# Kernel optimization log

Measured on AMD Instinct MI355X. Metric: run time of the kernel, lower is better.

## Reference

```python
import jax, jax.numpy as jnp
import numpy as np

B, L, DIM = 2, 1024, 512
HEADS = 8
D = DIM // HEADS
FORE_DIM, POST_DIM = 256, 1024
L_FORE, L_POST = 4 * L, L // 4


def setup_inputs() -> dict:
    key = jax.random.key(0)
    ks = jax.random.split(key, 8)
    s = 0.02  # weight init scale
    return {
        "x": jax.random.normal(ks[0], (B, L, DIM), jnp.float32),
        "fore_x": jax.random.normal(ks[1], (B, L_FORE, FORE_DIM), jnp.float32),
        "post_x": jax.random.normal(ks[2], (B, L_POST, POST_DIM), jnp.float32),
        # Linear weights stored [in, out] (transposed vs torch nn.Linear)
        "wq": jax.random.normal(ks[3], (DIM, DIM), jnp.float32) * s,
        "bq": jnp.zeros((DIM,), jnp.float32),
        "wkv1": jax.random.normal(ks[4], (FORE_DIM, 2 * DIM), jnp.float32) * s,
        "bkv1": jnp.zeros((2 * DIM,), jnp.float32),
        "wkv2": jax.random.normal(ks[5], (POST_DIM, 2 * DIM), jnp.float32) * s,
        "bkv2": jnp.zeros((2 * DIM,), jnp.float32),
        "wproj": jax.random.normal(ks[6], (3 * DIM, DIM), jnp.float32) * s,
        "bproj": jnp.zeros((DIM,), jnp.float32),
    }


def reference(x, fore_x, post_x, wq, bq, wkv1, bkv1, wkv2, bkv2, wproj, bproj):
    scale = D ** (-0.5)
    # q: [B, H, L, D], pre-scaled as in the torch code
    q = (x @ wq + bq).reshape(B, L, HEADS, D).transpose(0, 2, 1, 3) * scale

    def cross_attn(ctx, w, b):
        # ctx: [B, Lc, Cin] -> k, v: [B, H, Lc, D]
        kv = (ctx @ w + b).reshape(B, ctx.shape[1], 2, HEADS, D)
        k = kv[:, :, 0].transpose(0, 2, 1, 3)
        v = kv[:, :, 1].transpose(0, 2, 1, 3)
        attn = jax.nn.softmax(jnp.einsum("bhqd,bhkd->bhqk", q, k), axis=-1)
        out = jnp.einsum("bhqk,bhkd->bhqd", attn, v)
        return out.transpose(0, 2, 1, 3).reshape(B, L, DIM)

    x_2 = cross_attn(post_x, wkv2, bkv2)
    x_1 = cross_attn(fore_x, wkv1, bkv1)
    cat = jnp.concatenate([x, x_1, x_2], axis=2)  # [B, L, 3*DIM]
    return cat @ wproj + bproj
```

## Files before the change

kernel.cpp:

```cpp
#include <hip/hip_runtime.h>
#include <hip/hip_bf16.h>
#include <stdint.h>

typedef __attribute__((ext_vector_type(8))) short bf8;
typedef __attribute__((ext_vector_type(4))) short bf4;
typedef __attribute__((ext_vector_type(2))) short bf2;
typedef __attribute__((ext_vector_type(4))) float f32x4;

__device__ inline short f2bf(float f) {
  union { __hip_bfloat16 h; short s; } u;
  u.h = __float2bfloat16(f);
  return u.s;
}
__device__ inline float bf2f(short s) {
  union { short s; __hip_bfloat16 h; } u;
  u.s = s;
  return __bfloat162float(u.h);
}

__device__ inline f32x4 mfma16(bf8 a, bf8 b, f32x4 c) {
  return __builtin_amdgcn_mfma_f32_16x16x32_bf16(a, b, c, 0, 0, 0);
}

__global__ __launch_bounds__(256) void gemm3_k(
    const float* __restrict__ x, const float* __restrict__ fore,
    const float* __restrict__ post,
    const float* __restrict__ wq, const float* __restrict__ wkv1,
    const float* __restrict__ bkv1, const float* __restrict__ wkv2,
    short* __restrict__ kv1, short* __restrict__ cat,
    float* __restrict__ qpart, float* __restrict__ kv2part)
{
  __shared__ __align__(16) short a_lds[2][128 * 40];
  __shared__ __align__(16) short b_lds[2][64 * 40];

  const int bid = blockIdx.x;
  const float *A, *W, *bias = nullptr;
  void* out;
  int N, lda, ldo, m0, n0, koff;
  bool f32out, wcat = false;
  if (bid < 1024) {
    A = fore; W = wkv1; bias = bkv1; out = kv1;
    N = 1024; lda = 256; ldo = 1024; koff = 0;
    m0 = (bid >> 4) * 128; n0 = (bid & 15) * 64; f32out = false;
  } else if (bid < 1280) {
    int j = bid - 1024; int kc = j >> 7; j &= 127;
    A = x; W = wq; out = qpart + (size_t)kc * (2048 * 512);
    N = 512; lda = 512; ldo = 512; koff = kc * 256;
    m0 = (j >> 3) * 128; n0 = (j & 7) * 64; f32out = true;
    wcat = (j & 7) == 0;
  } else {
    int j = bid - 1280; int kc = j >> 6; j &= 63;
    A = post; W = wkv2; out = kv2part + (size_t)kc * (512 * 1024);
    N = 1024; lda = 1024; ldo = 1024; koff = kc * 256;
    m0 = (j >> 4) * 128; n0 = (j & 15) * 64; f32out = true;
  }

  const int tid = threadIdx.x;
  const int w = tid >> 6, lane = tid & 63, g = lane >> 4, lr = lane & 15;
  const int wrow = w & 1, wcol = w >> 1;

  f32x4 z = {0.f, 0.f, 0.f, 0.f};
  f32x4 acc[4][2];
#pragma unroll
  for (int mi = 0; mi < 4; ++mi)
#pragma unroll
    for (int ni = 0; ni < 2; ++ni) acc[mi][ni] = z;

  const int arow = tid >> 3, ac4 = tid & 7;
  const int bcol = tid & 63, bj4 = tid >> 6;

  float4 ra[4], rna[4];
  float rw[8], rnw[8];

  auto LOADA = [&](int kg, float4* af, float* wg) {
#pragma unroll
    for (int i = 0; i < 4; ++i)
      af[i] = *(const float4*)&A[(size_t)(m0 + arow + 32 * i) * lda + kg + ac4 * 4];
#pragma unroll
    for (int j = 0; j < 8; ++j)
      wg[j] = W[(size_t)(kg + bj4 * 8 + j) * N + n0 + bcol];
  };
  auto STAGE = [&](int b, const float4* af, const float* wg, int kg) {
#pragma unroll
    for (int i = 0; i < 4; ++i) {
      int rr = arow + 32 * i;
      int s = (ac4 >> 1) ^ (rr & 3);
      bf4 o;
      o[0] = f2bf(af[i].x); o[1] = f2bf(af[i].y);
      o[2] = f2bf(af[i].z); o[3] = f2bf(af[i].w);
      *(bf4*)&a_lds[b][rr * 40 + s * 8 + (ac4 & 1) * 4] = o;
      if (wcat)
        *(bf4*)&cat[(size_t)(m0 + rr) * 1536 + kg + ac4 * 4] = o;
    }
    int s = bj4 ^ (bcol & 3);
    bf8 o;
#pragma unroll
    for (int j = 0; j < 8; ++j) o[j] = f2bf(wg[j]);
    *(bf8*)&b_lds[b][bcol * 40 + s * 8] = o;
  };

  LOADA(koff, ra, rw);
  STAGE(0, ra, rw, koff);
  LOADA(koff + 32, rna, rnw);
  __syncthreads();

#pragma unroll
  for (int it = 0; it < 8; ++it) {
    if (it < 7) STAGE((it + 1) & 1, rna, rnw, koff + (it + 1) * 32);
    if (it < 6) LOADA(koff + (it + 2) * 32, rna, rnw);

    const int b = it & 1;
    bf8 afr[4], bfr[2];
#pragma unroll
    for (int mi = 0; mi < 4; ++mi) {
      int row = wrow * 64 + mi * 16 + lr;
      afr[mi] = *(const bf8*)&a_lds[b][row * 40 + ((g ^ (row & 3)) << 3)];
    }
#pragma unroll
    for (int ni = 0; ni < 2; ++ni) {
      int col = wcol * 32 + ni * 16 + lr;
      bfr[ni] = *(const bf8*)&b_lds[b][col * 40 + ((g ^ (col & 3)) << 3)];
    }
#pragma unroll
    for (int mi = 0; mi < 4; ++mi)
#pragma unroll
      for (int ni = 0; ni < 2; ++ni)
        acc[mi][ni] = mfma16(afr[mi], bfr[ni], acc[mi][ni]);
    __syncthreads();
  }

#pragma unroll
  for (int ni = 0; ni < 2; ++ni) {
    int col = n0 + wcol * 32 + ni * 16 + lr;
    float bv = f32out ? 0.f : bias[col];
#pragma unroll
    for (int mi = 0; mi < 4; ++mi) {
      int rowb = m0 + wrow * 64 + mi * 16 + g * 4;
#pragma unroll
      for (int r = 0; r < 4; ++r) {
        float val = acc[mi][ni][r] + bv;
        if (f32out)
          ((float*)out)[(size_t)(rowb + r) * ldo + col] = val;
        else
          ((short*)out)[(size_t)(rowb + r) * ldo + col] = f2bf(val);
      }
    }
  }
}

__global__ __launch_bounds__(256) void finalize_k(
    const float* __restrict__ qpart, const float* __restrict__ kv2part,
    const float* __restrict__ bq, const float* __restrict__ bkv2,
    short* __restrict__ qb, short* __restrict__ kv2)
{
  int i = blockIdx.x * 256 + threadIdx.x;
  if (i < 262144) {
    int col = (i * 4) & 511;
    float4 a = ((const float4*)qpart)[i];
    float4 b = ((const float4*)qpart)[i + 262144];
    float4 bv = *(const float4*)&bq[col];
    bf4 o;
    o[0] = f2bf((a.x + b.x + bv.x) * 0.125f);
    o[1] = f2bf((a.y + b.y + bv.y) * 0.125f);
    o[2] = f2bf((a.z + b.z + bv.z) * 0.125f);
    o[3] = f2bf((a.w + b.w + bv.w) * 0.125f);
    ((bf4*)qb)[i] = o;
  } else {
    int j = i - 262144;
    int col = (j * 4) & 1023;
    float4 a = ((const float4*)kv2part)[j];
    float4 b = ((const float4*)kv2part)[j + 131072];
    float4 c = ((const float4*)kv2part)[j + 262144];
    float4 d = ((const float4*)kv2part)[j + 393216];
    float4 bv = *(const float4*)&bkv2[col];
    bf4 o;
    o[0] = f2bf(a.x + b.x + c.x + d.x + bv.x);
    o[1] = f2bf(a.y + b.y + c.y + d.y + bv.y);
    o[2] = f2bf(a.z + b.z + c.z + d.z + bv.z);
    o[3] = f2bf(a.w + b.w + c.w + d.w + bv.w);
    ((bf4*)kv2)[j] = o;
  }
}

__global__ __launch_bounds__(256) void gemmo_k(
    const short* __restrict__ A, const float* __restrict__ W,
    const float* __restrict__ bias, float* __restrict__ out,
    int N, int K, int lda, int ldo)
{
  __shared__ __align__(16) short a_lds[2][64 * 40];
  __shared__ __align__(16) short b_lds[2][64 * 40];
  const int tid = threadIdx.x;
  const int w = tid >> 6, lane = tid & 63, g = lane >> 4, lr = lane & 15;
  const int m0 = blockIdx.x * 64, n0 = blockIdx.y * 64;

  f32x4 z = {0.f, 0.f, 0.f, 0.f};
  f32x4 acc[4];
#pragma unroll
  for (int mi = 0; mi < 4; ++mi) acc[mi] = z;

  const int arow = tid >> 2, ac8 = tid & 3;
  const int bcol = tid & 63, bj4 = tid >> 6;
  bf8 ra, rna;
  float rw[8], rnw[8];

  auto LOADA = [&](int kg, bf8& ab, float* wg) {
    ab = *(const bf8*)&A[(size_t)(m0 + arow) * lda + kg + ac8 * 8];
#pragma unroll
    for (int j = 0; j < 8; ++j)
      wg[j] = W[(size_t)(kg + bj4 * 8 + j) * N + n0 + bcol];
  };
  auto STAGE = [&](int b, bf8 ab, const float* wg) {
    *(bf8*)&a_lds[b][arow * 40 + ((ac8 ^ (arow & 3)) << 3)] = ab;
    int s = bj4 ^ (bcol & 3);
    bf8 o;
#pragma unroll
    for (int j = 0; j < 8; ++j) o[j] = f2bf(wg[j]);
    *(bf8*)&b_lds[b][bcol * 40 + s * 8] = o;
  };

  const int nit = K >> 5;
  LOADA(0, ra, rw);
  STAGE(0, ra, rw);
  LOADA(32, rna, rnw);
  __syncthreads();

  for (int it = 0; it < nit; ++it) {
    if (it + 1 < nit) STAGE((it + 1) & 1, rna, rnw);
    if (it + 2 < nit) LOADA((it + 2) * 32, rna, rnw);

    const int b = it & 1;
    bf8 afr[4], bfr;
#pragma unroll
    for (int mi = 0; mi < 4; ++mi) {
      int row = mi * 16 + lr;
      afr[mi] = *(const bf8*)&a_lds[b][row * 40 + ((g ^ (row & 3)) << 3)];
    }
    {
      int col = w * 16 + lr;
      bfr = *(const bf8*)&b_lds[b][col * 40 + ((g ^ (col & 3)) << 3)];
    }
#pragma unroll
    for (int mi = 0; mi < 4; ++mi) acc[mi] = mfma16(afr[mi], bfr, acc[mi]);
    __syncthreads();
  }

  {
    int col = n0 + w * 16 + lr;
    float bv = bias[col];
#pragma unroll
    for (int mi = 0; mi < 4; ++mi) {
      int rowb = m0 + mi * 16 + g * 4;
#pragma unroll
      for (int r = 0; r < 4; ++r)
        out[(size_t)(rowb + r) * ldo + col] = acc[mi][r] + bv;
    }
  }
}

__global__ __launch_bounds__(256) void attn_k(
    const short* __restrict__ q,
    const short* __restrict__ kv1, const short* __restrict__ kv2,
    short* __restrict__ o1, float* __restrict__ l1,
    short* __restrict__ o2, float* __restrict__ l2)
{
  __shared__ __align__(16) short k_lds[64 * 64];
  __shared__ __align__(16) short v_lds[64 * 72];
  const int tid = threadIdx.x;
  const int w = tid >> 6, lane = tid & 63, g = lane >> 4, lr = lane & 15;

  const int bid = blockIdx.x;
  const short* kvsrc;
  short* opart;
  float* lpart;
  int qt, h, bb, split, chunk, Lc;
  if (bid < 1024) {
    qt = bid & 7; h = (bid >> 3) & 7;
    int zz = bid >> 6; bb = zz >> 3; split = zz & 7;
    kvsrc = kv1; opart = o1; lpart = l1; chunk = 512; Lc = 4096;
  } else {
    int j = bid - 1024;
    qt = j & 7; h = (j >> 3) & 7;
    int zz = j >> 6; bb = zz >> 2; split = zz & 3;
    kvsrc = kv2; opart = o2; lpart = l2; chunk = 64; Lc = 256;
  }

  const int qbase = bb * 1024 + qt * 128 + w * 32;
  bf8 qfA[2], qfB[2];
#pragma unroll
  for (int s2 = 0; s2 < 2; ++s2) {
    const short* qp = &q[(size_t)(qbase + s2 * 16 + lr) * 512 + h * 64];
    qfA[s2] = *(const bf8*)&qp[g * 8];
    qfB[s2] = *(const bf8*)&qp[32 + g * 8];
  }

  const f32x4 z = {0.f, 0.f, 0.f, 0.f};
  f32x4 oaccT[2][4];
#pragma unroll
  for (int s2 = 0; s2 < 2; ++s2)
#pragma unroll
    for (int i = 0; i < 4; ++i) oaccT[s2][i] = z;
  float lsum_l[2] = {0.f, 0.f};

  const short* kvb = kvsrc + (size_t)bb * Lc * 1024 + (size_t)split * chunk * 1024;

  const int krow = tid >> 2, ksl = tid & 3;
  const short* kgp = kvb + (size_t)krow * 1024 + h * 64;
  const int vi = tid & 31, vj = tid >> 5;
  const short* vgp = kvb + (size_t)(2 * vi) * 1024 + 512 + h * 64 + vj * 8;
  const int lc0 = 2 * vi;
  const int vpos = (lc0 & 32) + ((lc0 & 12) << 1) + ((lc0 & 16) >> 2) + (lc0 & 3);

  bf8 k0c, k1c, v0c, v1c;
  k0c = *(const bf8*)(kgp + ksl * 8);
  k1c = *(const bf8*)(kgp + (ksl + 4) * 8);
  v0c = *(const bf8*)vgp;
  v1c = *(const bf8*)(vgp + 1024);

  const int nit = chunk >> 6;
  for (int it = 0; it < nit; ++it) {
    __syncthreads();
    *(bf8*)&k_lds[krow * 64 + ((ksl ^ (krow & 7)) << 3)] = k0c;
    *(bf8*)&k_lds[krow * 64 + (((ksl + 4) ^ (krow & 7)) << 3)] = k1c;
#pragma unroll
    for (int jj = 0; jj < 8; ++jj) {
      int d = vj * 8 + jj;
      bf2 pr; pr[0] = v0c[jj]; pr[1] = v1c[jj];
      *(bf2*)&v_lds[d * 72 + vpos] = pr;
    }
    __syncthreads();
    if (it + 1 < nit) {
      size_t off = (size_t)64 * 1024 * (it + 1);
      k0c = *(const bf8*)(kgp + off + ksl * 8);
      k1c = *(const bf8*)(kgp + off + (ksl + 4) * 8);
      v0c = *(const bf8*)(vgp + off);
      v1c = *(const bf8*)(vgp + off + 1024);
    }

    f32x4 sv[2][4];
#pragma unroll
    for (int t = 0; t < 4; ++t) {
      int lc = t * 16 + lr;
      bf8 kf0 = *(const bf8*)&k_lds[lc * 64 + ((g ^ (lc & 7)) << 3)];
      bf8 kf1 = *(const bf8*)&k_lds[lc * 64 + (((4 + g) ^ (lc & 7)) << 3)];
#pragma unroll
      for (int s2 = 0; s2 < 2; ++s2) {
        sv[s2][t] = mfma16(kf0, qfA[s2], z);
        sv[s2][t] = mfma16(kf1, qfB[s2], sv[s2][t]);
      }
    }

    bf8 pb[2][2];
#pragma unroll
    for (int s2 = 0; s2 < 2; ++s2) {
      float acc_l = 0.f;
#pragma unroll
      for (int t = 0; t < 4; ++t) {
        float p0 = __expf(sv[s2][t][0]);
        float p1 = __expf(sv[s2][t][1]);
        float p2 = __expf(sv[s2][t][2]);
        float p3 = __expf(sv[s2][t][3]);
        acc_l += (p0 + p1) + (p2 + p3);
        int c = t >> 1, hb = (t & 1) * 4;
        pb[s2][c][hb + 0] = f2bf(p0);
        pb[s2][c][hb + 1] = f2bf(p1);
        pb[s2][c][hb + 2] = f2bf(p2);
        pb[s2][c][hb + 3] = f2bf(p3);
      }
      lsum_l[s2] += acc_l;
    }

#pragma unroll
    for (int dt = 0; dt < 4; ++dt) {
      int d = dt * 16 + lr;
      bf8 vf0 = *(const bf8*)&v_lds[d * 72 + 8 * g];
      bf8 vf1 = *(const bf8*)&v_lds[d * 72 + 32 + 8 * g];
      oaccT[0][dt] = mfma16(vf0, pb[0][0], oaccT[0][dt]);
      oaccT[0][dt] = mfma16(vf1, pb[0][1], oaccT[0][dt]);
      oaccT[1][dt] = mfma16(vf0, pb[1][0], oaccT[1][dt]);
      oaccT[1][dt] = mfma16(vf1, pb[1][1], oaccT[1][dt]);
    }
  }

#pragma unroll
  for (int s2 = 0; s2 < 2; ++s2) {
    int prow = (bb * 8 + h) * 1024 + qt * 128 + w * 32 + s2 * 16 + lr;
    short* ob = opart + ((size_t)split * 16384 + prow) * 64;
#pragma unroll
    for (int dt = 0; dt < 4; ++dt) {
      bf4 o4;
#pragma unroll
      for (int r = 0; r < 4; ++r) o4[r] = f2bf(oaccT[s2][dt][r]);
      *(bf4*)&ob[dt * 16 + 4 * g] = o4;
    }
    float t = lsum_l[s2];
    t += __shfl_xor(t, 16);
    t += __shfl_xor(t, 32);
    if (g == 0) lpart[(size_t)split * 16384 + prow] = t;
  }
}

__global__ __launch_bounds__(256) void comb_k(
    const short* __restrict__ o1, const float* __restrict__ l1,
    const short* __restrict__ o2, const float* __restrict__ l2,
    short* __restrict__ cat)
{
  int row = blockIdx.x * 4 + (threadIdx.x >> 6);
  int d = threadIdx.x & 63;
  int bb = row >> 13, h = (row >> 10) & 7, qr = row & 1023;
  short* crow = &cat[(size_t)(bb * 1024 + qr) * 1536 + h * 64 + d];

  float o = 0.f, l = 0.f;
#pragma unroll
  for (int s = 0; s < 8; ++s) {
    o += bf2f(o1[((size_t)s * 16384 + row) * 64 + d]);
    l += l1[(size_t)s * 16384 + row];
  }
  crow[512] = f2bf(o / l);

  o = 0.f; l = 0.f;
#pragma unroll
  for (int s = 0; s < 4; ++s) {
    o += bf2f(o2[((size_t)s * 16384 + row) * 64 + d]);
    l += l2[(size_t)s * 16384 + row];
  }
  crow[1024] = f2bf(o / l);
}

extern "C" void kernel_launch(void* const* d_in, const int* in_sizes, int n_in,
                              void* d_out, int out_size, void* d_ws, size_t ws_size,
                              hipStream_t stream) {
  const float* x     = (const float*)d_in[0];
  const float* fore  = (const float*)d_in[1];
  const float* post  = (const float*)d_in[2];
  const float* wq    = (const float*)d_in[3];
  const float* bq    = (const float*)d_in[4];
  const float* wkv1  = (const float*)d_in[5];
  const float* bkv1  = (const float*)d_in[6];
  const float* wkv2  = (const float*)d_in[7];
  const float* bkv2  = (const float*)d_in[8];
  const float* wproj = (const float*)d_in[9];
  const float* bproj = (const float*)d_in[10];

  char* ws = (char*)d_ws;
  short* qb      = (short*)ws;
  short* kv1     = (short*)(ws + (2ull << 20));
  short* kv2     = (short*)(ws + (18ull << 20));
  short* cat     = (short*)(ws + (19ull << 20));
  short* o1      = (short*)(ws + (25ull << 20));
  short* o2      = (short*)(ws + (41ull << 20));
  float* l1      = (float*)(ws + (49ull << 20));
  float* l2      = (float*)(ws + (50ull << 20));
  float* qpart   = (float*)(ws + (51ull << 20));
  float* kv2part = (float*)(ws + (59ull << 20));

  gemm3_k<<<1536, 256, 0, stream>>>(x, fore, post, wq, wkv1, bkv1, wkv2,
                                    kv1, cat, qpart, kv2part);
  finalize_k<<<1536, 256, 0, stream>>>(qpart, kv2part, bq, bkv2, qb, kv2);
  attn_k<<<1536, 256, 0, stream>>>(qb, kv1, kv2, o1, l1, o2, l2);
  comb_k<<<4096, 256, 0, stream>>>(o1, l1, o2, l2, cat);
  gemmo_k<<<dim3(32, 8), 256, 0, stream>>>(cat, wproj, bproj, (float*)d_out,
                                           512, 1536, 1536, 512);
}
```

Before: 99.50 us.

## Store split-K partials in bf16, pre-transpose wproj, fold log2e into q scale

Split-K partial sums for q and kv2 are now written as bf16 instead of fp32, which halves the partial-sum traffic through finalize. Finalize also transposes wproj into a bf16 [N,K] layout, so the output GEMM loads both operands with one vector load each instead of eight strided fp32 loads plus conversion. Q is pre-scaled by log2(e) so attention can use exp2f, and the block orders in attention and the output GEMM are remapped to improve cache locality. Rounding the partials to bf16 before they are summed loses some precision, and the weight transpose runs on every call.

```diff
diff --git a/kernel.cpp b/kernel.cpp
--- a/kernel.cpp
+++ b/kernel.cpp
@@ -28,31 +28,31 @@
     const float* __restrict__ wq, const float* __restrict__ wkv1,
     const float* __restrict__ bkv1, const float* __restrict__ wkv2,
     short* __restrict__ kv1, short* __restrict__ cat,
-    float* __restrict__ qpart, float* __restrict__ kv2part)
+    short* __restrict__ qpart, short* __restrict__ kv2part)
 {
   __shared__ __align__(16) short a_lds[2][128 * 40];
   __shared__ __align__(16) short b_lds[2][64 * 40];
 
   const int bid = blockIdx.x;
   const float *A, *W, *bias = nullptr;
-  void* out;
+  short* out;
   int N, lda, ldo, m0, n0, koff;
-  bool f32out, wcat = false;
+  bool addb, wcat = false;
   if (bid < 1024) {
     A = fore; W = wkv1; bias = bkv1; out = kv1;
     N = 1024; lda = 256; ldo = 1024; koff = 0;
-    m0 = (bid >> 4) * 128; n0 = (bid & 15) * 64; f32out = false;
+    m0 = (bid >> 4) * 128; n0 = (bid & 15) * 64; addb = true;
   } else if (bid < 1280) {
     int j = bid - 1024; int kc = j >> 7; j &= 127;
     A = x; W = wq; out = qpart + (size_t)kc * (2048 * 512);
     N = 512; lda = 512; ldo = 512; koff = kc * 256;
-    m0 = (j >> 3) * 128; n0 = (j & 7) * 64; f32out = true;
+    m0 = (j >> 3) * 128; n0 = (j & 7) * 64; addb = false;
     wcat = (j & 7) == 0;
   } else {
     int j = bid - 1280; int kc = j >> 6; j &= 63;
     A = post; W = wkv2; out = kv2part + (size_t)kc * (512 * 1024);
     N = 1024; lda = 1024; ldo = 1024; koff = kc * 256;
-    m0 = (j >> 4) * 128; n0 = (j & 15) * 64; f32out = true;
+    m0 = (j >> 4) * 128; n0 = (j & 15) * 64; addb = false;
   }
 
   const int tid = threadIdx.x;
@@ -132,66 +132,86 @@
 #pragma unroll
   for (int ni = 0; ni < 2; ++ni) {
     int col = n0 + wcol * 32 + ni * 16 + lr;
-    float bv = f32out ? 0.f : bias[col];
+    float bv = addb ? bias[col] : 0.f;
 #pragma unroll
     for (int mi = 0; mi < 4; ++mi) {
       int rowb = m0 + wrow * 64 + mi * 16 + g * 4;
 #pragma unroll
-      for (int r = 0; r < 4; ++r) {
-        float val = acc[mi][ni][r] + bv;
-        if (f32out)
-          ((float*)out)[(size_t)(rowb + r) * ldo + col] = val;
-        else
-          ((short*)out)[(size_t)(rowb + r) * ldo + col] = f2bf(val);
-      }
+      for (int r = 0; r < 4; ++r)
+        out[(size_t)(rowb + r) * ldo + col] = f2bf(acc[mi][ni][r] + bv);
     }
   }
 }
 
 __global__ __launch_bounds__(256) void finalize_k(
-    const float* __restrict__ qpart, const float* __restrict__ kv2part,
+    const short* __restrict__ qpart, const short* __restrict__ kv2part,
     const float* __restrict__ bq, const float* __restrict__ bkv2,
-    short* __restrict__ qb, short* __restrict__ kv2)
+    const float* __restrict__ wproj,
+    short* __restrict__ qb, short* __restrict__ kv2, short* __restrict__ wT)
 {
-  int i = blockIdx.x * 256 + threadIdx.x;
-  if (i < 262144) {
+  __shared__ float tl[64][65];
+  const int bid = blockIdx.x, tid = threadIdx.x;
+  if (bid < 1024) {
+    int i = bid * 256 + tid;
+    const float qsc = 0.125f * 1.44269504088896f;
+    bf4 a = *(const bf4*)&qpart[(size_t)i * 4];
+    bf4 b = *(const bf4*)&qpart[1048576 + (size_t)i * 4];
     int col = (i * 4) & 511;
-    float4 a = ((const float4*)qpart)[i];
-    float4 b = ((const float4*)qpart)[i + 262144];
-    float4 bv = *(const float4*)&bq[col];
     bf4 o;
-    o[0] = f2bf((a.x + b.x + bv.x) * 0.125f);
-    o[1] = f2bf((a.y + b.y + bv.y) * 0.125f);
-    o[2] = f2bf((a.z + b.z + bv.z) * 0.125f);
-    o[3] = f2bf((a.w + b.w + bv.w) * 0.125f);
+#pragma unroll
+    for (int j = 0; j < 4; ++j)
+      o[j] = f2bf((bf2f(a[j]) + bf2f(b[j]) + bq[col + j]) * qsc);
     ((bf4*)qb)[i] = o;
+  } else if (bid < 1536) {
+    int i = (bid - 1024) * 256 + tid;
+    bf4 a = *(const bf4*)&kv2part[(size_t)i * 4];
+    bf4 b = *(const bf4*)&kv2part[524288 + (size_t)i * 4];
+    bf4 c = *(const bf4*)&kv2part[1048576 + (size_t)i * 4];
+    bf4 d = *(const bf4*)&kv2part[1572864 + (size_t)i * 4];
+    int col = (i * 4) & 1023;
+    bf4 o;
+#pragma unroll
+    for (int j = 0; j < 4; ++j)
+      o[j] = f2bf(bf2f(a[j]) + bf2f(b[j]) + bf2f(c[j]) + bf2f(d[j]) + bkv2[col + j]);
+    ((bf4*)kv2)[i] = o;
   } else {
-    int j = i - 262144;
-    int col = (j * 4) & 1023;
-    float4 a = ((const float4*)kv2part)[j];
-    float4 b = ((const float4*)kv2part)[j + 131072];
-    float4 c = ((const float4*)kv2part)[j + 262144];
-    float4 d = ((const float4*)kv2part)[j + 393216];
-    float4 bv = *(const float4*)&bkv2[col];
-    bf4 o;
-    o[0] = f2bf(a.x + b.x + c.x + d.x + bv.x);
-    o[1] = f2bf(a.y + b.y + c.y + d.y + bv.y);
-    o[2] = f2bf(a.z + b.z + c.z + d.z + bv.z);
-    o[3] = f2bf(a.w + b.w + c.w + d.w + bv.w);
-    ((bf4*)kv2)[j] = o;
+    int tb = bid - 1536;
+    int kt = tb % 24, nt = tb / 24;
+    int k0 = kt * 64, n0 = nt * 64;
+    int kr = tid >> 2, c4 = tid & 3;
+#pragma unroll
+    for (int i = 0; i < 4; ++i) {
+      int cc = c4 + i * 4;
+      float4 v = *(const float4*)&wproj[(size_t)(k0 + kr) * 512 + n0 + cc * 4];
+      tl[kr][cc * 4 + 0] = v.x; tl[kr][cc * 4 + 1] = v.y;
+      tl[kr][cc * 4 + 2] = v.z; tl[kr][cc * 4 + 3] = v.w;
+    }
+    __syncthreads();
+    int nr = tid >> 2, p = tid & 3;
+#pragma unroll
+    for (int i = 0; i < 2; ++i) {
+      int kk = p * 16 + i * 8;
+      bf8 o;
+#pragma unroll
+      for (int j = 0; j < 8; ++j) o[j] = f2bf(tl[kk + j][nr]);
+      *(bf8*)&wT[(size_t)(n0 + nr) * 1536 + k0 + kk] = o;
+    }
   }
 }
 
 __global__ __launch_bounds__(256) void gemmo_k(
-    const short* __restrict__ A, const float* __restrict__ W,
-    const float* __restrict__ bias, float* __restrict__ out,
-    int N, int K, int lda, int ldo)
+    const short* __restrict__ A, const short* __restrict__ wT,
+    const float* __restrict__ bias, float* __restrict__ out)
 {
   __shared__ __align__(16) short a_lds[2][64 * 40];
   __shared__ __align__(16) short b_lds[2][64 * 40];
   const int tid = threadIdx.x;
   const int w = tid >> 6, lane = tid & 63, g = lane >> 4, lr = lane & 15;
-  const int m0 = blockIdx.x * 64, n0 = blockIdx.y * 64;
+  const int id = blockIdx.x;
+  const int m = ((id >> 3) & 3) | ((id & 7) << 2);
+  const int n = id >> 5;
+  const int m0 = m * 64, n0 = n * 64;
+  const int K = 1536, N = 512;
 
   f32x4 z = {0.f, 0.f, 0.f, 0.f};
   f32x4 acc[4];
@@ -200,33 +220,26 @@
 
   const int arow = tid >> 2, ac8 = tid & 3;
   const int bcol = tid & 63, bj4 = tid >> 6;
-  bf8 ra, rna;
-  float rw[8], rnw[8];
-
-  auto LOADA = [&](int kg, bf8& ab, float* wg) {
-    ab = *(const bf8*)&A[(size_t)(m0 + arow) * lda + kg + ac8 * 8];
-#pragma unroll
-    for (int j = 0; j < 8; ++j)
-      wg[j] = W[(size_t)(kg + bj4 * 8 + j) * N + n0 + bcol];
+  bf8 ra, rna, rb, rnb;
+
+  auto LOADAB = [&](int kg, bf8& ab, bf8& bb) {
+    ab = *(const bf8*)&A[(size_t)(m0 + arow) * K + kg + ac8 * 8];
+    bb = *(const bf8*)&wT[(size_t)(n0 + bcol) * K + kg + bj4 * 8];
   };
-  auto STAGE = [&](int b, bf8 ab, const float* wg) {
+  auto STAGE = [&](int b, bf8 ab, bf8 bb) {
     *(bf8*)&a_lds[b][arow * 40 + ((ac8 ^ (arow & 3)) << 3)] = ab;
-    int s = bj4 ^ (bcol & 3);
-    bf8 o;
-#pragma unroll
-    for (int j = 0; j < 8; ++j) o[j] = f2bf(wg[j]);
-    *(bf8*)&b_lds[b][bcol * 40 + s * 8] = o;
+    *(bf8*)&b_lds[b][bcol * 40 + ((bj4 ^ (bcol & 3)) << 3)] = bb;
   };
 
   const int nit = K >> 5;
-  LOADA(0, ra, rw);
-  STAGE(0, ra, rw);
-  LOADA(32, rna, rnw);
+  LOADAB(0, ra, rb);
+  STAGE(0, ra, rb);
+  LOADAB(32, rna, rnb);
   __syncthreads();
 
   for (int it = 0; it < nit; ++it) {
-    if (it + 1 < nit) STAGE((it + 1) & 1, rna, rnw);
-    if (it + 2 < nit) LOADA((it + 2) * 32, rna, rnw);
+    if (it + 1 < nit) STAGE((it + 1) & 1, rna, rnb);
+    if (it + 2 < nit) LOADAB((it + 2) * 32, rna, rnb);
 
     const int b = it & 1;
     bf8 afr[4], bfr;
@@ -252,7 +265,7 @@
       int rowb = m0 + mi * 16 + g * 4;
 #pragma unroll
       for (int r = 0; r < 4; ++r)
-        out[(size_t)(rowb + r) * ldo + col] = acc[mi][r] + bv;
+        out[(size_t)(rowb + r) * 512 + col] = acc[mi][r] + bv;
     }
   }
 }
@@ -274,13 +287,15 @@
   float* lpart;
   int qt, h, bb, split, chunk, Lc;
   if (bid < 1024) {
-    qt = bid & 7; h = (bid >> 3) & 7;
-    int zz = bid >> 6; bb = zz >> 3; split = zz & 7;
+    qt = bid >> 7; int j = bid & 127;
+    h = j & 7; int zz = j >> 3;
+    bb = zz >> 3; split = zz & 7;
     kvsrc = kv1; opart = o1; lpart = l1; chunk = 512; Lc = 4096;
   } else {
-    int j = bid - 1024;
-    qt = j & 7; h = (j >> 3) & 7;
-    int zz = j >> 6; bb = zz >> 2; split = zz & 3;
+    int j2 = bid - 1024;
+    qt = j2 >> 6; int r = j2 & 63;
+    h = r & 7; int zz = r >> 3;
+    bb = zz >> 2; split = zz & 3;
     kvsrc = kv2; opart = o2; lpart = l2; chunk = 64; Lc = 256;
   }
 
@@ -355,10 +370,10 @@
       float acc_l = 0.f;
 #pragma unroll
       for (int t = 0; t < 4; ++t) {
-        float p0 = __expf(sv[s2][t][0]);
-        float p1 = __expf(sv[s2][t][1]);
-        float p2 = __expf(sv[s2][t][2]);
-        float p3 = __expf(sv[s2][t][3]);
+        float p0 = exp2f(sv[s2][t][0]);
+        float p1 = exp2f(sv[s2][t][1]);
+        float p2 = exp2f(sv[s2][t][2]);
+        float p3 = exp2f(sv[s2][t][3]);
         acc_l += (p0 + p1) + (p2 + p3);
         int c = t >> 1, hb = (t & 1) * 4;
         pb[s2][c][hb + 0] = f2bf(p0);
@@ -449,15 +464,16 @@
   short* o1      = (short*)(ws + (25ull << 20));
   short* o2      = (short*)(ws + (41ull << 20));
   float* l1      = (float*)(ws + (49ull << 20));
-  float* l2      = (float*)(ws + (50ull << 20));
-  float* qpart   = (float*)(ws + (51ull << 20));
-  float* kv2part = (float*)(ws + (59ull << 20));
+  float* l2      = (float*)(ws + (49ull << 20) + 524288);
+  short* qpart   = (short*)(ws + (50ull << 20));
+  short* kv2part = (short*)(ws + (52ull << 20));
+  short* wT      = (short*)(ws + (56ull << 20));
 
   gemm3_k<<<1536, 256, 0, stream>>>(x, fore, post, wq, wkv1, bkv1, wkv2,
                                     kv1, cat, qpart, kv2part);
-  finalize_k<<<1536, 256, 0, stream>>>(qpart, kv2part, bq, bkv2, qb, kv2);
+  finalize_k<<<1728, 256, 0, stream>>>(qpart, kv2part, bq, bkv2, wproj,
+                                       qb, kv2, wT);
   attn_k<<<1536, 256, 0, stream>>>(qb, kv1, kv2, o1, l1, o2, l2);
   comb_k<<<4096, 256, 0, stream>>>(o1, l1, o2, l2, cat);
-  gemmo_k<<<dim3(32, 8), 256, 0, stream>>>(cat, wproj, bproj, (float*)d_out,
-                                           512, 1536, 1536, 512);
-}
+  gemmo_k<<<256, 256, 0, stream>>>(cat, wT, bproj, (float*)d_out);
+}
```

New measurement: 91.20 us. -8.3%, faster.
